# Kernel tuning notes

Hardware: AMD Instinct MI355X
Metric: run time of the kernel (lower is better)

## Reference

```python
import jax, jax.numpy as jnp
import numpy as np

ALPHA = 0.2  # LeakyReLU negative slope


def setup_inputs() -> dict:
    key = jax.random.key(0)
    k1, k2, k3, k4 = jax.random.split(key, 4)
    N, IN, OUT = 8192, 512, 256
    x = jax.random.normal(k1, (N, IN), dtype=jnp.float32)
    adj = jnp.zeros((N, N), dtype=jnp.float32)  # accepted but unused by the module
    W = jax.random.normal(k2, (OUT, IN), dtype=jnp.float32) * (1.0 / np.sqrt(IN))
    a1 = jax.random.normal(k3, (OUT,), dtype=jnp.float32) * (1.0 / np.sqrt(OUT))
    a2 = jax.random.normal(k4, (OUT,), dtype=jnp.float32) * (1.0 / np.sqrt(OUT))
    return {"x": x, "adj": adj, "W": W, "a1": a1, "a2": a2}


def reference(x, adj, W, a1, a2):
    # h = tran(x): [N, OUT]
    h = x @ W.T
    # additive GAT scores: e[i, j] = a2 . h_i + a1 . h_j  (from unsqueeze(0)+unsqueeze(1))
    s1 = h @ a1  # [N], att1(h)
    s2 = h @ a2  # [N], att2(h)
    e = s2[:, None] + s1[None, :]  # [N, N]
    e = jnp.where(e > 0, e, ALPHA * e)  # LeakyReLU
    attn = jax.nn.softmax(e, axis=1)  # softmax over dim=1; dropout is identity in eval
    return attn @ h  # [N, OUT]
```

## Files before the change

kernel.cpp:

```cpp
#include <hip/hip_runtime.h>

#define NROW 8192
#define DIN  512
#define DOUT 256
#define NCHUNK 1024
#define CLEN 8
#define NGRP 32
#define GLEN 32
#define JCH 8

constexpr size_t OFF_H      = 0;
constexpr size_t OFF_S1     = OFF_H + (size_t)NROW*DOUT*4;
constexpr size_t OFF_S2     = OFF_S1 + NROW*4;
constexpr size_t OFF_RANK   = OFF_S2 + NROW*4;
constexpr size_t OFF_GLO    = OFF_RANK + NROW*4;
constexpr size_t OFF_GHI    = OFF_GLO + (size_t)NGRP*DOUT*4;
constexpr size_t OFF_GSLO   = OFF_GHI + (size_t)NGRP*DOUT*4;
constexpr size_t OFF_GSHI   = OFF_GSLO + 128;
constexpr size_t MEMSET_LEN = OFF_GSHI + 128 - OFF_S1;
constexpr size_t OFF_S1S    = OFF_GSHI + 128;
constexpr size_t OFF_PERM   = OFF_S1S + NROW*4;
constexpr size_t OFF_WHI    = OFF_PERM + NROW*4;
constexpr size_t OFF_WLO    = OFF_WHI + NROW*4;
constexpr size_t OFF_PRELOS = OFF_WLO + NROW*4;
constexpr size_t OFF_SUFHIS = OFF_PRELOS + 33024;
constexpr size_t OFF_CSLO   = OFF_SUFHIS + 33024;
constexpr size_t OFF_CSHI   = OFF_CSLO + (size_t)NCHUNK*4;
constexpr size_t OFF_TLO    = OFF_CSHI + (size_t)NCHUNK*4;
constexpr size_t OFF_THI    = OFF_TLO + (size_t)NCHUNK*DOUT*4;
constexpr size_t OFF_PRELO  = OFF_THI + (size_t)NCHUNK*DOUT*4;
constexpr size_t OFF_SUFHI  = OFF_PRELO + (size_t)(NROW+1)*DOUT*4;
constexpr size_t WS_NEED    = OFF_SUFHI + (size_t)(NROW+1)*DOUT*4;

__global__ __launch_bounds__(256) void gemm_h(const float* __restrict__ x,
                                              const float* __restrict__ W,
                                              const float* __restrict__ a1,
                                              const float* __restrict__ a2,
                                              float* __restrict__ h,
                                              float* __restrict__ s1,
                                              float* __restrict__ s2) {
  __shared__ float xs[64][68];
  __shared__ float ws[64][68];
  const int tid = threadIdx.x;
  const int rowBase = blockIdx.x * 64;
  const int colBase = blockIdx.y * 64;
  const int ty = tid >> 4, tx = tid & 15;
  float acc[4][4] = {};
  for (int k0 = 0; k0 < DIN; k0 += 64) {
#pragma unroll
    for (int i = 0; i < 4; ++i) {
      int s = i * 256 + tid;
      int r = s >> 4;
      int kk = (s & 15) << 2;
      float4 v = *(const float4*)(x + (size_t)(rowBase + r) * DIN + k0 + kk);
      xs[kk + 0][r] = v.x; xs[kk + 1][r] = v.y; xs[kk + 2][r] = v.z; xs[kk + 3][r] = v.w;
      float4 u = *(const float4*)(W + (size_t)(colBase + r) * DIN + k0 + kk);
      ws[kk + 0][r] = u.x; ws[kk + 1][r] = u.y; ws[kk + 2][r] = u.z; ws[kk + 3][r] = u.w;
    }
    __syncthreads();
#pragma unroll
    for (int kk = 0; kk < 64; ++kk) {
      float4 av = *(const float4*)&xs[kk][ty << 2];
      float4 bv = *(const float4*)&ws[kk][tx << 2];
      float a[4] = {av.x, av.y, av.z, av.w};
      float b[4] = {bv.x, bv.y, bv.z, bv.w};
#pragma unroll
      for (int r = 0; r < 4; ++r)
#pragma unroll
        for (int c = 0; c < 4; ++c) acc[r][c] = fmaf(a[r], b[c], acc[r][c]);
    }
    __syncthreads();
  }
#pragma unroll
  for (int r = 0; r < 4; ++r) {
    float4 o = make_float4(acc[r][0], acc[r][1], acc[r][2], acc[r][3]);
    *(float4*)(h + (size_t)(rowBase + (ty << 2) + r) * DOUT + colBase + (tx << 2)) = o;
  }
  float4 A1 = *(const float4*)(a1 + colBase + (tx << 2));
  float4 A2 = *(const float4*)(a2 + colBase + (tx << 2));
#pragma unroll
  for (int r = 0; r < 4; ++r) {
    float p1 = acc[r][0] * A1.x + acc[r][1] * A1.y + acc[r][2] * A1.z + acc[r][3] * A1.w;
    float p2 = acc[r][0] * A2.x + acc[r][1] * A2.y + acc[r][2] * A2.z + acc[r][3] * A2.w;
#pragma unroll
    for (int m = 1; m < 16; m <<= 1) {
      p1 += __shfl_xor(p1, m);
      p2 += __shfl_xor(p2, m);
    }
    if (tx == 0) {
      int row = rowBase + (ty << 2) + r;
      atomicAdd(&s1[row], p1);
      atomicAdd(&s2[row], p2);
    }
  }
}

__global__ __launch_bounds__(256) void rank_count(const float* __restrict__ s1,
                                                  int* __restrict__ rank) {
  __shared__ float sj[1024];
  const int t = threadIdx.x;
  const int ib = blockIdx.x, jc = blockIdx.y;
  const int j0 = jc * 1024;
  *(float4*)&sj[t << 2] = *(const float4*)(s1 + j0 + (t << 2));
  const int i = ib * 256 + t;
  const float v = s1[i];
  __syncthreads();
  int cnt = 0;
#pragma unroll 4
  for (int q = 0; q < 256; ++q) {
    float4 sv = *(const float4*)&sj[q << 2];
    int jg = j0 + (q << 2);
    cnt += (int)(sv.x < v) + (int)((sv.x == v) & (jg + 0 < i));
    cnt += (int)(sv.y < v) + (int)((sv.y == v) & (jg + 1 < i));
    cnt += (int)(sv.z < v) + (int)((sv.z == v) & (jg + 2 < i));
    cnt += (int)(sv.w < v) + (int)((sv.w == v) & (jg + 3 < i));
  }
  atomicAdd(&rank[i], cnt);
}

__global__ __launch_bounds__(256) void scatter_w(const float* __restrict__ s1,
                                                 const int* __restrict__ rank,
                                                 float* __restrict__ s1s,
                                                 int* __restrict__ perm,
                                                 float* __restrict__ w_hi,
                                                 float* __restrict__ w_lo) {
  const int i = blockIdx.x * 256 + threadIdx.x;
  const float v = s1[i];
  const int r = rank[i];
  s1s[r] = v;
  perm[r] = i;
  w_hi[r] = __expf(v);
  w_lo[r] = __expf(0.2f * v);
}

__global__ __launch_bounds__(256) void chunk_totals(const float* __restrict__ h,
                                                    const int* __restrict__ perm,
                                                    const float* __restrict__ w_hi,
                                                    const float* __restrict__ w_lo,
                                                    float* __restrict__ T_lo,
                                                    float* __restrict__ T_hi,
                                                    float* __restrict__ G_lo,
                                                    float* __restrict__ G_hi,
                                                    float* __restrict__ cs_lo,
                                                    float* __restrict__ cs_hi,
                                                    float* __restrict__ GS_lo,
                                                    float* __restrict__ GS_hi) {
  const int d = threadIdx.x, c = blockIdx.x, g = c >> 5;
  const int j0 = c * CLEN;
  float tlo = 0.f, thi = 0.f;
#pragma unroll
  for (int e = 0; e < CLEN; e += 4) {
    int4 p4 = *(const int4*)(perm + j0 + e);
    float4 wl4 = *(const float4*)(w_lo + j0 + e);
    float4 wh4 = *(const float4*)(w_hi + j0 + e);
    float h0 = h[(size_t)p4.x * DOUT + d];
    float h1 = h[(size_t)p4.y * DOUT + d];
    float h2 = h[(size_t)p4.z * DOUT + d];
    float h3 = h[(size_t)p4.w * DOUT + d];
    tlo += wl4.x * h0 + wl4.y * h1 + wl4.z * h2 + wl4.w * h3;
    thi += wh4.x * h0 + wh4.y * h1 + wh4.z * h2 + wh4.w * h3;
  }
  T_lo[c * DOUT + d] = tlo;
  T_hi[c * DOUT + d] = thi;
  atomicAdd(&G_lo[g * DOUT + d], tlo);
  atomicAdd(&G_hi[g * DOUT + d], thi);
  if (d < 64) {
    float wl = (d < CLEN) ? w_lo[j0 + d] : 0.f;
    float wh = (d < CLEN) ? w_hi[j0 + d] : 0.f;
#pragma unroll
    for (int off = 4; off > 0; off >>= 1) {
      wl += __shfl_down(wl, off);
      wh += __shfl_down(wh, off);
    }
    if (d == 0) {
      cs_lo[c] = wl; cs_hi[c] = wh;
      atomicAdd(&GS_lo[g], wl); atomicAdd(&GS_hi[g], wh);
    }
  }
}

__global__ __launch_bounds__(256) void write_prefix(const float* __restrict__ h,
                                                    const int* __restrict__ perm,
                                                    const float* __restrict__ w_hi,
                                                    const float* __restrict__ w_lo,
                                                    const float* __restrict__ T_lo,
                                                    const float* __restrict__ T_hi,
                                                    const float* __restrict__ G_lo,
                                                    const float* __restrict__ G_hi,
                                                    const float* __restrict__ cs_lo,
                                                    const float* __restrict__ cs_hi,
                                                    const float* __restrict__ GS_lo,
                                                    const float* __restrict__ GS_hi,
                                                    float* __restrict__ PreLo,
                                                    float* __restrict__ SufHi,
                                                    float* __restrict__ prelo_s,
                                                    float* __restrict__ sufhi_s) {
  const int d = threadIdx.x, c = blockIdx.x;
  const int g = c >> 5, cin = c & 31;
  const int j0 = c * CLEN;
  if (d < 64) {
    float sp = 0.f, st = 0.f;
    if (d < 32) {
      float gl = GS_lo[d], gh = GS_hi[d];
      float cl = cs_lo[g * GLEN + d], ch = cs_hi[g * GLEN + d];
      sp = ((d < g) ? gl : 0.f) + ((d < cin) ? cl : 0.f);
      st = ((d > g) ? gh : 0.f) + ((d > cin) ? ch : 0.f);
    }
#pragma unroll
    for (int off = 32; off > 0; off >>= 1) {
      sp += __shfl_down(sp, off);
      st += __shfl_down(st, off);
    }
    float pres  = __shfl(sp, 0);
    float tails = __shfl(st, 0);
    float wl = (d < CLEN) ? w_lo[j0 + d] : 0.f;
    float wh = (d < CLEN) ? w_hi[j0 + d] : 0.f;
    float pl = wl, ph = wh;
#pragma unroll
    for (int off = 1; off < CLEN; off <<= 1) {
      float a = __shfl_up(pl, off);
      float b = __shfl_up(ph, off);
      if (d >= off) { pl += a; ph += b; }
    }
    float tot = __shfl(ph, CLEN - 1);
    if (d < CLEN) {
      prelo_s[j0 + d] = pres + (pl - wl);
      sufhi_s[j0 + d] = tails + tot - ph + wh;
    }
    if (c == NCHUNK - 1 && d == CLEN - 1) {
      prelo_s[NROW] = pres + pl;
      sufhi_s[NROW] = 0.f;
    }
  }
  float rl = 0.f, tail = 0.f;
#pragma unroll 8
  for (int p = 0; p < NGRP; ++p) {
    float gl = G_lo[p * DOUT + d];
    float gh = G_hi[p * DOUT + d];
    rl   += (p < g) ? gl : 0.f;
    tail += (p > g) ? gh : 0.f;
  }
  const int cbase = g * GLEN;
#pragma unroll 8
  for (int q = 0; q < GLEN; ++q) {
    float vl = T_lo[(cbase + q) * DOUT + d];
    float vh = T_hi[(cbase + q) * DOUT + d];
    rl   += (q < cin) ? vl : 0.f;
    tail += (q > cin) ? vh : 0.f;
  }
  float hv[CLEN], wlv[CLEN], whv[CLEN];
  float ownHi = 0.f;
#pragma unroll
  for (int e = 0; e < CLEN; e += 4) {
    int4 p4 = *(const int4*)(perm + j0 + e);
    float4 wl4 = *(const float4*)(w_lo + j0 + e);
    float4 wh4 = *(const float4*)(w_hi + j0 + e);
    hv[e + 0] = h[(size_t)p4.x * DOUT + d];
    hv[e + 1] = h[(size_t)p4.y * DOUT + d];
    hv[e + 2] = h[(size_t)p4.z * DOUT + d];
    hv[e + 3] = h[(size_t)p4.w * DOUT + d];
    wlv[e + 0] = wl4.x; wlv[e + 1] = wl4.y; wlv[e + 2] = wl4.z; wlv[e + 3] = wl4.w;
    whv[e + 0] = wh4.x; whv[e + 1] = wh4.y; whv[e + 2] = wh4.z; whv[e + 3] = wh4.w;
    ownHi += wh4.x * hv[e] + wh4.y * hv[e + 1] + wh4.z * hv[e + 2] + wh4.w * hv[e + 3];
  }
  float shb = tail + ownHi;
  float preh = 0.f;
#pragma unroll
  for (int e = 0; e < CLEN; ++e) {
    size_t j = (size_t)(j0 + e);
    PreLo[j * DOUT + d] = rl;
    SufHi[j * DOUT + d] = shb - preh;
    rl   += wlv[e] * hv[e];
    preh += whv[e] * hv[e];
  }
  if (c == NCHUNK - 1) {
    PreLo[(size_t)NROW * DOUT + d] = rl;
    SufHi[(size_t)NROW * DOUT + d] = 0.f;
  }
}

__global__ __launch_bounds__(256) void finalize(const float* __restrict__ s2,
                                                const float* __restrict__ s1s,
                                                const float* __restrict__ PreLo,
                                                const float* __restrict__ SufHi,
                                                const float* __restrict__ prelo_s,
                                                const float* __restrict__ sufhi_s,
                                                float* __restrict__ out) {
  const int wave = threadIdx.x >> 6, lane = threadIdx.x & 63;
  const int i = blockIdx.x * 4 + wave;
  const float c = s2[i];
  const float tval = -c;
  int lo = 0, hi = NROW;
  while (lo < hi) {
    int mid = (lo + hi) >> 1;
    if (s1s[mid] <= tval) lo = mid + 1; else hi = mid;
  }
  const int k = lo;
  const float fh = __expf(c);
  const float fl = __expf(0.2f * c);
  const float den = fh * sufhi_s[k] + fl * prelo_s[k];
  const float inv = 1.f / den;
  float4 A = *(const float4*)(SufHi + (size_t)k * DOUT + (lane << 2));
  float4 B = *(const float4*)(PreLo + (size_t)k * DOUT + (lane << 2));
  float4 o;
  o.x = (fh * A.x + fl * B.x) * inv;
  o.y = (fh * A.y + fl * B.y) * inv;
  o.z = (fh * A.z + fl * B.z) * inv;
  o.w = (fh * A.w + fl * B.w) * inv;
  *(float4*)(out + (size_t)i * DOUT + (lane << 2)) = o;
}

extern "C" void kernel_launch(void* const* d_in, const int* in_sizes, int n_in,
                              void* d_out, int out_size, void* d_ws, size_t ws_size,
                              hipStream_t stream) {
  const float* x  = (const float*)d_in[0];
  const float* W  = (const float*)d_in[2];
  const float* a1 = (const float*)d_in[3];
  const float* a2 = (const float*)d_in[4];
  float* out = (float*)d_out;

  char* ws = (char*)d_ws;
  if (ws_size < WS_NEED) ws = (char*)d_in[1];

  float* h       = (float*)(ws + OFF_H);
  float* s1      = (float*)(ws + OFF_S1);
  float* s2      = (float*)(ws + OFF_S2);
  int*   rank    = (int*)  (ws + OFF_RANK);
  float* G_lo    = (float*)(ws + OFF_GLO);
  float* G_hi    = (float*)(ws + OFF_GHI);
  float* GS_lo   = (float*)(ws + OFF_GSLO);
  float* GS_hi   = (float*)(ws + OFF_GSHI);
  float* s1s     = (float*)(ws + OFF_S1S);
  int*   perm    = (int*)  (ws + OFF_PERM);
  float* w_hi    = (float*)(ws + OFF_WHI);
  float* w_lo    = (float*)(ws + OFF_WLO);
  float* prelo_s = (float*)(ws + OFF_PRELOS);
  float* sufhi_s = (float*)(ws + OFF_SUFHIS);
  float* cs_lo   = (float*)(ws + OFF_CSLO);
  float* cs_hi   = (float*)(ws + OFF_CSHI);
  float* T_lo    = (float*)(ws + OFF_TLO);
  float* T_hi    = (float*)(ws + OFF_THI);
  float* PreLo   = (float*)(ws + OFF_PRELO);
  float* SufHi   = (float*)(ws + OFF_SUFHI);

  hipMemsetAsync(s1, 0, MEMSET_LEN, stream);

  gemm_h<<<dim3(NROW / 64, DOUT / 64), 256, 0, stream>>>(x, W, a1, a2, h, s1, s2);
  rank_count<<<dim3(NROW / 256, JCH), 256, 0, stream>>>(s1, rank);
  scatter_w<<<NROW / 256, 256, 0, stream>>>(s1, rank, s1s, perm, w_hi, w_lo);
  chunk_totals<<<NCHUNK, 256, 0, stream>>>(h, perm, w_hi, w_lo, T_lo, T_hi,
                                           G_lo, G_hi, cs_lo, cs_hi, GS_lo, GS_hi);
  write_prefix<<<NCHUNK, 256, 0, stream>>>(h, perm, w_hi, w_lo, T_lo, T_hi,
                                           G_lo, G_hi, cs_lo, cs_hi, GS_lo, GS_hi,
                                           PreLo, SufHi, prelo_s, sufhi_s);
  finalize<<<NROW / 4, 256, 0, stream>>>(s2, s1s, PreLo, SufHi, prelo_s, sufhi_s, out);
}
```

Measured before the change: 406.8 us.

## Fuse prefix writing and finalize by bucketing queries per sorted-key chunk

Instead of materialising full PreLo/SufHi prefix tables (two 8193x256 float arrays) and then binary-searching per output row, queries are also ranked (by s2 descending and by their threshold position in sorted s1), so each chunk block directly emits output rows for the queries whose split point falls inside its chunk. This removes roughly 16 MB of prefix-table writes and reads plus the separate finalize kernel. The cost is extra counting work in rank_count, two binary searches per block, and uneven per-block work when many queries land in one chunk; the query ranking by s2 serves only to group same-chunk queries.

```diff
diff --git a/kernel.cpp b/kernel.cpp
--- a/kernel.cpp
+++ b/kernel.cpp
@@ -12,25 +12,25 @@
 constexpr size_t OFF_H      = 0;
 constexpr size_t OFF_S1     = OFF_H + (size_t)NROW*DOUT*4;
 constexpr size_t OFF_S2     = OFF_S1 + NROW*4;
-constexpr size_t OFF_RANK   = OFF_S2 + NROW*4;
-constexpr size_t OFF_GLO    = OFF_RANK + NROW*4;
+constexpr size_t OFF_RK1    = OFF_S2 + NROW*4;
+constexpr size_t OFF_KRK    = OFF_RK1 + NROW*4;
+constexpr size_t OFF_RK2    = OFF_KRK + NROW*4;
+constexpr size_t OFF_GLO    = OFF_RK2 + NROW*4;
 constexpr size_t OFF_GHI    = OFF_GLO + (size_t)NGRP*DOUT*4;
 constexpr size_t OFF_GSLO   = OFF_GHI + (size_t)NGRP*DOUT*4;
 constexpr size_t OFF_GSHI   = OFF_GSLO + 128;
 constexpr size_t MEMSET_LEN = OFF_GSHI + 128 - OFF_S1;
-constexpr size_t OFF_S1S    = OFF_GSHI + 128;
-constexpr size_t OFF_PERM   = OFF_S1S + NROW*4;
+constexpr size_t OFF_PERM   = OFF_GSHI + 128;
 constexpr size_t OFF_WHI    = OFF_PERM + NROW*4;
 constexpr size_t OFF_WLO    = OFF_WHI + NROW*4;
-constexpr size_t OFF_PRELOS = OFF_WLO + NROW*4;
-constexpr size_t OFF_SUFHIS = OFF_PRELOS + 33024;
-constexpr size_t OFF_CSLO   = OFF_SUFHIS + 33024;
+constexpr size_t OFF_S2S    = OFF_WLO + NROW*4;
+constexpr size_t OFF_QPERM  = OFF_S2S + NROW*4;
+constexpr size_t OFF_KSORT  = OFF_QPERM + NROW*4;
+constexpr size_t OFF_CSLO   = OFF_KSORT + NROW*4;
 constexpr size_t OFF_CSHI   = OFF_CSLO + (size_t)NCHUNK*4;
 constexpr size_t OFF_TLO    = OFF_CSHI + (size_t)NCHUNK*4;
 constexpr size_t OFF_THI    = OFF_TLO + (size_t)NCHUNK*DOUT*4;
-constexpr size_t OFF_PRELO  = OFF_THI + (size_t)NCHUNK*DOUT*4;
-constexpr size_t OFF_SUFHI  = OFF_PRELO + (size_t)(NROW+1)*DOUT*4;
-constexpr size_t WS_NEED    = OFF_SUFHI + (size_t)(NROW+1)*DOUT*4;
+constexpr size_t WS_NEED    = OFF_THI + (size_t)NCHUNK*DOUT*4;
 
 __global__ __launch_bounds__(256) void gemm_h(const float* __restrict__ x,
                                               const float* __restrict__ W,
@@ -96,41 +96,64 @@
 }
 
 __global__ __launch_bounds__(256) void rank_count(const float* __restrict__ s1,
-                                                  int* __restrict__ rank) {
-  __shared__ float sj[1024];
+                                                  const float* __restrict__ s2,
+                                                  int* __restrict__ rank1,
+                                                  int* __restrict__ krank,
+                                                  int* __restrict__ rank2) {
+  __shared__ float sj1[1024];
+  __shared__ float sj2[1024];
   const int t = threadIdx.x;
   const int ib = blockIdx.x, jc = blockIdx.y;
   const int j0 = jc * 1024;
-  *(float4*)&sj[t << 2] = *(const float4*)(s1 + j0 + (t << 2));
+  *(float4*)&sj1[t << 2] = *(const float4*)(s1 + j0 + (t << 2));
+  *(float4*)&sj2[t << 2] = *(const float4*)(s2 + j0 + (t << 2));
   const int i = ib * 256 + t;
-  const float v = s1[i];
+  const float v1 = s1[i];
+  const float s2i = s2[i];
+  const float v2m = -s2i;
   __syncthreads();
-  int cnt = 0;
+  int c1 = 0, ck = 0, c2 = 0;
 #pragma unroll 4
   for (int q = 0; q < 256; ++q) {
-    float4 sv = *(const float4*)&sj[q << 2];
+    float4 a = *(const float4*)&sj1[q << 2];
+    float4 b = *(const float4*)&sj2[q << 2];
     int jg = j0 + (q << 2);
-    cnt += (int)(sv.x < v) + (int)((sv.x == v) & (jg + 0 < i));
-    cnt += (int)(sv.y < v) + (int)((sv.y == v) & (jg + 1 < i));
-    cnt += (int)(sv.z < v) + (int)((sv.z == v) & (jg + 2 < i));
-    cnt += (int)(sv.w < v) + (int)((sv.w == v) & (jg + 3 < i));
-  }
-  atomicAdd(&rank[i], cnt);
+    c1 += (int)(a.x < v1) + (int)((a.x == v1) & (jg + 0 < i));
+    c1 += (int)(a.y < v1) + (int)((a.y == v1) & (jg + 1 < i));
+    c1 += (int)(a.z < v1) + (int)((a.z == v1) & (jg + 2 < i));
+    c1 += (int)(a.w < v1) + (int)((a.w == v1) & (jg + 3 < i));
+    ck += (int)(a.x <= v2m) + (int)(a.y <= v2m) + (int)(a.z <= v2m) + (int)(a.w <= v2m);
+    c2 += (int)(b.x > s2i) + (int)((b.x == s2i) & (jg + 0 < i));
+    c2 += (int)(b.y > s2i) + (int)((b.y == s2i) & (jg + 1 < i));
+    c2 += (int)(b.z > s2i) + (int)((b.z == s2i) & (jg + 2 < i));
+    c2 += (int)(b.w > s2i) + (int)((b.w == s2i) & (jg + 3 < i));
+  }
+  atomicAdd(&rank1[i], c1);
+  atomicAdd(&krank[i], ck);
+  atomicAdd(&rank2[i], c2);
 }
 
 __global__ __launch_bounds__(256) void scatter_w(const float* __restrict__ s1,
-                                                 const int* __restrict__ rank,
-                                                 float* __restrict__ s1s,
+                                                 const float* __restrict__ s2,
+                                                 const int* __restrict__ rank1,
+                                                 const int* __restrict__ krank,
+                                                 const int* __restrict__ rank2,
                                                  int* __restrict__ perm,
                                                  float* __restrict__ w_hi,
-                                                 float* __restrict__ w_lo) {
+                                                 float* __restrict__ w_lo,
+                                                 int* __restrict__ qperm,
+                                                 int* __restrict__ ksort,
+                                                 float* __restrict__ s2s) {
   const int i = blockIdx.x * 256 + threadIdx.x;
   const float v = s1[i];
-  const int r = rank[i];
-  s1s[r] = v;
-  perm[r] = i;
-  w_hi[r] = __expf(v);
-  w_lo[r] = __expf(0.2f * v);
+  const int r1 = rank1[i];
+  perm[r1] = i;
+  w_hi[r1] = __expf(v);
+  w_lo[r1] = __expf(0.2f * v);
+  const int r2 = rank2[i];
+  qperm[r2] = i;
+  ksort[r2] = krank[i];
+  s2s[r2] = s2[i];
 }
 
 __global__ __launch_bounds__(256) void chunk_totals(const float* __restrict__ h,
@@ -179,22 +202,31 @@
   }
 }
 
-__global__ __launch_bounds__(256) void write_prefix(const float* __restrict__ h,
-                                                    const int* __restrict__ perm,
-                                                    const float* __restrict__ w_hi,
-                                                    const float* __restrict__ w_lo,
-                                                    const float* __restrict__ T_lo,
-                                                    const float* __restrict__ T_hi,
-                                                    const float* __restrict__ G_lo,
-                                                    const float* __restrict__ G_hi,
-                                                    const float* __restrict__ cs_lo,
-                                                    const float* __restrict__ cs_hi,
-                                                    const float* __restrict__ GS_lo,
-                                                    const float* __restrict__ GS_hi,
-                                                    float* __restrict__ PreLo,
-                                                    float* __restrict__ SufHi,
-                                                    float* __restrict__ prelo_s,
-                                                    float* __restrict__ sufhi_s) {
+__device__ __forceinline__ int lb8192(const int* __restrict__ a, int target) {
+  int pos = 0;
+#pragma unroll
+  for (int b = 4096; b > 0; b >>= 1)
+    if (a[pos + b - 1] < target) pos += b;
+  return pos;
+}
+
+__global__ __launch_bounds__(256) void emit_out(const float* __restrict__ h,
+                                                const int* __restrict__ perm,
+                                                const float* __restrict__ w_hi,
+                                                const float* __restrict__ w_lo,
+                                                const float* __restrict__ T_lo,
+                                                const float* __restrict__ T_hi,
+                                                const float* __restrict__ G_lo,
+                                                const float* __restrict__ G_hi,
+                                                const float* __restrict__ cs_lo,
+                                                const float* __restrict__ cs_hi,
+                                                const float* __restrict__ GS_lo,
+                                                const float* __restrict__ GS_hi,
+                                                const int* __restrict__ qperm,
+                                                const int* __restrict__ ksort,
+                                                const float* __restrict__ s2s,
+                                                float* __restrict__ out) {
+  __shared__ float sh_sc[2];
   const int d = threadIdx.x, c = blockIdx.x;
   const int g = c >> 5, cin = c & 31;
   const int j0 = c * CLEN;
@@ -211,26 +243,7 @@
       sp += __shfl_down(sp, off);
       st += __shfl_down(st, off);
     }
-    float pres  = __shfl(sp, 0);
-    float tails = __shfl(st, 0);
-    float wl = (d < CLEN) ? w_lo[j0 + d] : 0.f;
-    float wh = (d < CLEN) ? w_hi[j0 + d] : 0.f;
-    float pl = wl, ph = wh;
-#pragma unroll
-    for (int off = 1; off < CLEN; off <<= 1) {
-      float a = __shfl_up(pl, off);
-      float b = __shfl_up(ph, off);
-      if (d >= off) { pl += a; ph += b; }
-    }
-    float tot = __shfl(ph, CLEN - 1);
-    if (d < CLEN) {
-      prelo_s[j0 + d] = pres + (pl - wl);
-      sufhi_s[j0 + d] = tails + tot - ph + wh;
-    }
-    if (c == NCHUNK - 1 && d == CLEN - 1) {
-      prelo_s[NROW] = pres + pl;
-      sufhi_s[NROW] = 0.f;
-    }
+    if (d == 0) { sh_sc[0] = sp; sh_sc[1] = st; }
   }
   float rl = 0.f, tail = 0.f;
 #pragma unroll 8
@@ -249,7 +262,7 @@
     tail += (q > cin) ? vh : 0.f;
   }
   float hv[CLEN], wlv[CLEN], whv[CLEN];
-  float ownHi = 0.f;
+  float ownHi = 0.f, ownHiS = 0.f;
 #pragma unroll
   for (int e = 0; e < CLEN; e += 4) {
     int4 p4 = *(const int4*)(perm + j0 + e);
@@ -262,52 +275,41 @@
     wlv[e + 0] = wl4.x; wlv[e + 1] = wl4.y; wlv[e + 2] = wl4.z; wlv[e + 3] = wl4.w;
     whv[e + 0] = wh4.x; whv[e + 1] = wh4.y; whv[e + 2] = wh4.z; whv[e + 3] = wh4.w;
     ownHi += wh4.x * hv[e] + wh4.y * hv[e + 1] + wh4.z * hv[e + 2] + wh4.w * hv[e + 3];
-  }
-  float shb = tail + ownHi;
-  float preh = 0.f;
+    ownHiS += wh4.x + wh4.y + wh4.z + wh4.w;
+  }
+  __syncthreads();
+  const float pres = sh_sc[0], tails = sh_sc[1];
+  const int qlo = lb8192(ksort, j0);
+  int qhi = lb8192(ksort, j0 + CLEN);
+  float pre_v = rl, suf_v = tail + ownHi;
+  float pre_sc = pres, suf_sc = tails + ownHiS;
+  int q = qlo;
 #pragma unroll
   for (int e = 0; e < CLEN; ++e) {
-    size_t j = (size_t)(j0 + e);
-    PreLo[j * DOUT + d] = rl;
-    SufHi[j * DOUT + d] = shb - preh;
-    rl   += wlv[e] * hv[e];
-    preh += whv[e] * hv[e];
+    const int kb = j0 + e;
+    while (q < qhi && ksort[q] == kb) {
+      const int iq = qperm[q];
+      const float c2 = s2s[q];
+      const float fh = __expf(c2);
+      const float fl = __expf(0.2f * c2);
+      const float inv = 1.f / (fh * suf_sc + fl * pre_sc);
+      out[(size_t)iq * DOUT + d] = (fh * suf_v + fl * pre_v) * inv;
+      ++q;
+    }
+    pre_v += wlv[e] * hv[e];  suf_v -= whv[e] * hv[e];
+    pre_sc += w_lo[j0 + e];   suf_sc -= whv[e];
   }
   if (c == NCHUNK - 1) {
-    PreLo[(size_t)NROW * DOUT + d] = rl;
-    SufHi[(size_t)NROW * DOUT + d] = 0.f;
-  }
-}
-
-__global__ __launch_bounds__(256) void finalize(const float* __restrict__ s2,
-                                                const float* __restrict__ s1s,
-                                                const float* __restrict__ PreLo,
-                                                const float* __restrict__ SufHi,
-                                                const float* __restrict__ prelo_s,
-                                                const float* __restrict__ sufhi_s,
-                                                float* __restrict__ out) {
-  const int wave = threadIdx.x >> 6, lane = threadIdx.x & 63;
-  const int i = blockIdx.x * 4 + wave;
-  const float c = s2[i];
-  const float tval = -c;
-  int lo = 0, hi = NROW;
-  while (lo < hi) {
-    int mid = (lo + hi) >> 1;
-    if (s1s[mid] <= tval) lo = mid + 1; else hi = mid;
-  }
-  const int k = lo;
-  const float fh = __expf(c);
-  const float fl = __expf(0.2f * c);
-  const float den = fh * sufhi_s[k] + fl * prelo_s[k];
-  const float inv = 1.f / den;
-  float4 A = *(const float4*)(SufHi + (size_t)k * DOUT + (lane << 2));
-  float4 B = *(const float4*)(PreLo + (size_t)k * DOUT + (lane << 2));
-  float4 o;
-  o.x = (fh * A.x + fl * B.x) * inv;
-  o.y = (fh * A.y + fl * B.y) * inv;
-  o.z = (fh * A.z + fl * B.z) * inv;
-  o.w = (fh * A.w + fl * B.w) * inv;
-  *(float4*)(out + (size_t)i * DOUT + (lane << 2)) = o;
+    while (q < NROW) {
+      const int iq = qperm[q];
+      const float c2 = s2s[q];
+      const float fh = __expf(c2);
+      const float fl = __expf(0.2f * c2);
+      const float inv = 1.f / (fh * suf_sc + fl * pre_sc);
+      out[(size_t)iq * DOUT + d] = (fh * suf_v + fl * pre_v) * inv;
+      ++q;
+    }
+  }
 }
 
 extern "C" void kernel_launch(void* const* d_in, const int* in_sizes, int n_in,
@@ -322,36 +324,36 @@
   char* ws = (char*)d_ws;
   if (ws_size < WS_NEED) ws = (char*)d_in[1];
 
-  float* h       = (float*)(ws + OFF_H);
-  float* s1      = (float*)(ws + OFF_S1);
-  float* s2      = (float*)(ws + OFF_S2);
-  int*   rank    = (int*)  (ws + OFF_RANK);
-  float* G_lo    = (float*)(ws + OFF_GLO);
-  float* G_hi    = (float*)(ws + OFF_GHI);
-  float* GS_lo   = (float*)(ws + OFF_GSLO);
-  float* GS_hi   = (float*)(ws + OFF_GSHI);
-  float* s1s     = (float*)(ws + OFF_S1S);
-  int*   perm    = (int*)  (ws + OFF_PERM);
-  float* w_hi    = (float*)(ws + OFF_WHI);
-  float* w_lo    = (float*)(ws + OFF_WLO);
-  float* prelo_s = (float*)(ws + OFF_PRELOS);
-  float* sufhi_s = (float*)(ws + OFF_SUFHIS);
-  float* cs_lo   = (float*)(ws + OFF_CSLO);
-  float* cs_hi   = (float*)(ws + OFF_CSHI);
-  float* T_lo    = (float*)(ws + OFF_TLO);
-  float* T_hi    = (float*)(ws + OFF_THI);
-  float* PreLo   = (float*)(ws + OFF_PRELO);
-  float* SufHi   = (float*)(ws + OFF_SUFHI);
+  float* h     = (float*)(ws + OFF_H);
+  float* s1    = (float*)(ws + OFF_S1);
+  float* s2    = (float*)(ws + OFF_S2);
+  int*   rank1 = (int*)  (ws + OFF_RK1);
+  int*   krank = (int*)  (ws + OFF_KRK);
+  int*   rank2 = (int*)  (ws + OFF_RK2);
+  float* G_lo  = (float*)(ws + OFF_GLO);
+  float* G_hi  = (float*)(ws + OFF_GHI);
+  float* GS_lo = (float*)(ws + OFF_GSLO);
+  float* GS_hi = (float*)(ws + OFF_GSHI);
+  int*   perm  = (int*)  (ws + OFF_PERM);
+  float* w_hi  = (float*)(ws + OFF_WHI);
+  float* w_lo  = (float*)(ws + OFF_WLO);
+  float* s2s   = (float*)(ws + OFF_S2S);
+  int*   qperm = (int*)  (ws + OFF_QPERM);
+  int*   ksort = (int*)  (ws + OFF_KSORT);
+  float* cs_lo = (float*)(ws + OFF_CSLO);
+  float* cs_hi = (float*)(ws + OFF_CSHI);
+  float* T_lo  = (float*)(ws + OFF_TLO);
+  float* T_hi  = (float*)(ws + OFF_THI);
 
   hipMemsetAsync(s1, 0, MEMSET_LEN, stream);
 
   gemm_h<<<dim3(NROW / 64, DOUT / 64), 256, 0, stream>>>(x, W, a1, a2, h, s1, s2);
-  rank_count<<<dim3(NROW / 256, JCH), 256, 0, stream>>>(s1, rank);
-  scatter_w<<<NROW / 256, 256, 0, stream>>>(s1, rank, s1s, perm, w_hi, w_lo);
+  rank_count<<<dim3(NROW / 256, JCH), 256, 0, stream>>>(s1, s2, rank1, krank, rank2);
+  scatter_w<<<NROW / 256, 256, 0, stream>>>(s1, s2, rank1, krank, rank2,
+                                            perm, w_hi, w_lo, qperm, ksort, s2s);
   chunk_totals<<<NCHUNK, 256, 0, stream>>>(h, perm, w_hi, w_lo, T_lo, T_hi,
                                            G_lo, G_hi, cs_lo, cs_hi, GS_lo, GS_hi);
-  write_prefix<<<NCHUNK, 256, 0, stream>>>(h, perm, w_hi, w_lo, T_lo, T_hi,
-                                           G_lo, G_hi, cs_lo, cs_hi, GS_lo, GS_hi,
-                                           PreLo, SufHi, prelo_s, sufhi_s);
-  finalize<<<NROW / 4, 256, 0, stream>>>(s2, s1s, PreLo, SufHi, prelo_s, sufhi_s, out);
-}
+  emit_out<<<NCHUNK, 256, 0, stream>>>(h, perm, w_hi, w_lo, T_lo, T_hi,
+                                       G_lo, G_hi, cs_lo, cs_hi, GS_lo, GS_hi,
+                                       qperm, ksort, s2s, out);
+}
```

Result: slower. 426.0 us (+4.7%).
